# Optimization experiments

Hardware: AMD Instinct MI355X
Metric: run time of the kernel (lower is better)

## Reference

```python
import jax, jax.numpy as jnp
import numpy as np

GROUPS = 32
HEADS = 8
EPS = 1e-5

def setup_inputs() -> dict:
    key = jax.random.key(0)
    ks = jax.random.split(key, 5)
    C = 512
    x = jax.random.normal(ks[0], (8, C, 32, 32), dtype=jnp.float32)
    gn_w = jnp.ones((C,), dtype=jnp.float32)
    gn_b = jnp.zeros((C,), dtype=jnp.float32)
    qkv_w = jax.random.normal(ks[1], (3 * C, C), dtype=jnp.float32) * 0.02
    qkv_b = jnp.zeros((3 * C,), dtype=jnp.float32)
    proj_w = jax.random.normal(ks[2], (C, C), dtype=jnp.float32) * 0.02
    proj_b = jnp.zeros((C,), dtype=jnp.float32)
    return {"x": x, "gn_w": gn_w, "gn_b": gn_b, "qkv_w": qkv_w,
            "qkv_b": qkv_b, "proj_w": proj_w, "proj_b": proj_b}

def reference(x, gn_w, gn_b, qkv_w, qkv_b, proj_w, proj_b):
    B, C, H, W = x.shape
    d = C // HEADS
    # GroupNorm(32, C)
    xg = x.reshape(B, GROUPS, C // GROUPS, H, W)
    mean = xg.mean(axis=(2, 3, 4), keepdims=True)
    var = xg.var(axis=(2, 3, 4), keepdims=True)
    h = ((xg - mean) * jax.lax.rsqrt(var + EPS)).reshape(B, C, H, W)
    h = h * gn_w[None, :, None, None] + gn_b[None, :, None, None]
    # 1x1 conv QKV == channel matmul
    qkv = jnp.einsum('bchw,oc->bohw', h, qkv_w) + qkv_b[None, :, None, None]
    qkv = qkv.reshape(B, 3, HEADS, d, H * W)
    q, k, v = qkv[:, 0], qkv[:, 1], qkv[:, 2]  # [B, heads, d, HW]
    scale = d ** (-0.5)
    # weight[b,h,q,k] = sum_d q[b,h,d,q] * k[b,h,d,k] * scale
    attn = jax.nn.softmax(jnp.einsum('bhdq,bhdk->bhqk', q, k) * scale, axis=-1)
    # out[b,h,d,q] = sum_k v[b,h,d,k] * attn[b,h,q,k]
    out = jnp.einsum('bhdk,bhqk->bhdq', v, attn).reshape(B, C, H, W)
    out = jnp.einsum('bchw,oc->bohw', out, proj_w) + proj_b[None, :, None, None]
    return out + x
```

## Files before the change

### kernel.cpp

```cpp
#include <hip/hip_runtime.h>
#include <math.h>

#define B_    8
#define C_    512
#define HW_   1024
#define O3_   1536
#define HEADS_ 8
#define D_    64
#define G_    32
#define CPG_  16
#define EPS_  1e-5f
#define M_TOT 8192

#define QSCALE (0.125f * 1.44269504088896f)

typedef __bf16 bf16x8 __attribute__((ext_vector_type(8)));
typedef __bf16 bf16x4 __attribute__((ext_vector_type(4)));
typedef float  f32x4  __attribute__((ext_vector_type(4)));

__device__ __forceinline__ void async_copy16(void* lds, const void* g) {
  __builtin_amdgcn_global_load_lds(
      (const __attribute__((address_space(1))) unsigned int*)g,
      (__attribute__((address_space(3))) unsigned int*)lds, 16, 0, 0);
}

__global__ __launch_bounds__(256) void k_gn(const float* __restrict__ x,
                                            const float* __restrict__ gw,
                                            const float* __restrict__ gb,
                                            __bf16* __restrict__ h,
                                            const float* __restrict__ qw,
                                            const float* __restrict__ pw,
                                            __bf16* __restrict__ qwb,
                                            __bf16* __restrict__ pwb) {
  __shared__ float red[10];
  __shared__ __bf16 T[16 * 1030];
  if (blockIdx.x >= B_ * G_) {
    int i = (blockIdx.x - B_ * G_) * 256 + threadIdx.x;
    if (i < O3_ * C_) qwb[i] = (__bf16)qw[i];
    if (i < C_ * C_)  pwb[i] = (__bf16)pw[i];
    return;
  }
  int bg = blockIdx.x;
  int b = bg >> 5, g = bg & 31;
  const float* xg = x + ((size_t)(b * C_) + g * CPG_) * HW_;
  int tid = threadIdx.x;

  float s = 0.f, ss = 0.f;
  for (int i = tid; i < CPG_ * HW_; i += 256) {
    float v = xg[i];
    s += v; ss += v * v;
  }
  for (int off = 32; off > 0; off >>= 1) {
    s  += __shfl_down(s, off, 64);
    ss += __shfl_down(ss, off, 64);
  }
  int wv = tid >> 6;
  if ((tid & 63) == 0) { red[wv] = s; red[4 + wv] = ss; }
  __syncthreads();
  if (tid == 0) {
    float S  = red[0] + red[1] + red[2] + red[3];
    float SS = red[4] + red[5] + red[6] + red[7];
    float mean = S / (float)(CPG_ * HW_);
    float var  = SS / (float)(CPG_ * HW_) - mean * mean;
    red[8] = mean;
    red[9] = rsqrtf(var + EPS_);
  }
  __syncthreads();
  float mean = red[8], rstd = red[9];

  for (int i = tid; i < CPG_ * HW_; i += 256) {
    int c = i >> 10, hw = i & 1023;
    float ga = gw[g * CPG_ + c], be = gb[g * CPG_ + c];
    float v = xg[i];
    T[c * 1030 + hw] = (__bf16)((v - mean) * rstd * ga + be);
  }
  __syncthreads();

  __bf16* hb = h + (size_t)b * HW_ * C_ + g * CPG_;
  for (int j = tid; j < CPG_ * HW_; j += 256) {
    int hw = j >> 4, c = j & 15;
    hb[(size_t)hw * C_ + c] = T[c * 1030 + hw];
  }
}

#define BK 64
__device__ __forceinline__ void gemm128_core(const __bf16* __restrict__ aBase,
                                             const __bf16* __restrict__ bBase,
                                             __bf16* As, __bf16* Bs,
                                             f32x4 acc[4][4]) {
  int t = threadIdx.x;
  int lane = t & 63;
  int l16 = lane & 15, quad = lane >> 4;
  int wv = t >> 6;
  int wm = (wv >> 1) * 64, wn = (wv & 1) * 64;

  int rsub = lane >> 3;
  int chunk = (lane & 7) ^ rsub;
  const __bf16* ag = aBase + (size_t)(wv * 32 + rsub) * C_ + chunk * 8;
  const __bf16* bg = bBase + (size_t)(wv * 32 + rsub) * C_ + chunk * 8;
  __bf16* la = As + wv * 2048 + lane * 8;
  __bf16* lb = Bs + wv * 2048 + lane * 8;
  int sw = l16 & 7;

  for (int k0 = 0; k0 < C_; k0 += BK) {
#pragma unroll
    for (int s = 0; s < 4; s++) {
      async_copy16(la + s * 512, ag + (size_t)(s * 8) * C_ + k0);
      async_copy16(lb + s * 512, bg + (size_t)(s * 8) * C_ + k0);
    }
    __syncthreads();
#pragma unroll
    for (int h = 0; h < 2; h++) {
      bf16x8 af[4], bf[4];
#pragma unroll
      for (int i = 0; i < 4; i++) {
        af[i] = *(const bf16x8*)(As + (wm + i * 16 + l16) * BK +
                                 ((h * 4 + quad) ^ sw) * 8);
        bf[i] = *(const bf16x8*)(Bs + (wn + i * 16 + l16) * BK +
                                 ((h * 4 + quad) ^ sw) * 8);
      }
#pragma unroll
      for (int i = 0; i < 4; i++)
#pragma unroll
        for (int j = 0; j < 4; j++)
          acc[i][j] = __builtin_amdgcn_mfma_f32_16x16x32_bf16(af[i], bf[j],
                                                              acc[i][j], 0, 0, 0);
    }
    __syncthreads();
  }
}

__global__ __launch_bounds__(256) void k_qkv(const __bf16* __restrict__ h,
                                             const __bf16* __restrict__ w,
                                             const float* __restrict__ bias,
                                             __bf16* __restrict__ y,
                                             __bf16* __restrict__ vT) {
  __shared__ __align__(16) __bf16 As[128 * BK];
  __shared__ __align__(16) __bf16 Bs[128 * BK];
  int m0 = blockIdx.x * 128, n0 = blockIdx.y * 128;
  f32x4 acc[4][4];
#pragma unroll
  for (int i = 0; i < 4; i++)
#pragma unroll
    for (int j = 0; j < 4; j++) acc[i][j] = f32x4{0.f, 0.f, 0.f, 0.f};
  gemm128_core(h + (size_t)m0 * C_, w + (size_t)n0 * C_, As, Bs, acc);

  int lane = threadIdx.x & 63, wv = threadIdx.x >> 6;
  int l16 = lane & 15, quad = lane >> 4;
  int wm = (wv >> 1) * 64, wn = (wv & 1) * 64;

  if (n0 >= 2 * C_) {
    int bb = m0 >> 10;
    int tokBase = (m0 & 1023) + wm + quad * 4;
#pragma unroll
    for (int j = 0; j < 4; j++) {
      int n = n0 + wn + j * 16 + l16;
      int c = n - 2 * C_;
      float bv = bias[n];
      __bf16* vrow = vT + ((size_t)(bb * C_) + c) * HW_;
#pragma unroll
      for (int i = 0; i < 4; i++) {
        bf16x4 pk;
#pragma unroll
        for (int r = 0; r < 4; r++) pk[r] = (__bf16)(acc[i][j][r] + bv);
        *(bf16x4*)(vrow + tokBase + i * 16) = pk;
      }
    }
  } else {
    float sc = (n0 < C_) ? QSCALE : 1.0f;
#pragma unroll
    for (int j = 0; j < 4; j++) {
      int n = n0 + wn + j * 16 + l16;
      float bv = bias[n];
#pragma unroll
      for (int i = 0; i < 4; i++)
#pragma unroll
        for (int r = 0; r < 4; r++) {
          int m = m0 + wm + i * 16 + quad * 4 + r;
          y[(size_t)m * O3_ + n] = (__bf16)((acc[i][j][r] + bv) * sc);
        }
    }
  }
}

__global__ __launch_bounds__(256) void k_attn(const __bf16* __restrict__ y,
                                              const __bf16* __restrict__ vT,
                                              __bf16* __restrict__ ao) {
  __shared__ __align__(16) __bf16 Ks[128 * 64];
  __shared__ __align__(16) __bf16 Vt[64 * 128];
  __shared__ __align__(16) __bf16 Pp[4][32 * 136];
  int hd = blockIdx.x, b = blockIdx.y, qt = blockIdx.z;
  int t = threadIdx.x;
  int wv = t >> 6, lane = t & 63, l16 = lane & 15, quad = lane >> 4;
  int q0 = qt * 128 + wv * 32;

  const __bf16* base = y + (size_t)(b * HW_) * O3_ + hd * D_;
  const __bf16* kg = base + C_;
  const __bf16* vtg = vT + ((size_t)(b * C_) + hd * D_) * HW_;

  bf16x8 qb[2][2];
#pragma unroll
  for (int qg = 0; qg < 2; qg++)
#pragma unroll
    for (int dh = 0; dh < 2; dh++)
      qb[qg][dh] = *(const bf16x8*)(base + (size_t)(q0 + qg * 16 + l16) * O3_ +
                                    dh * 32 + quad * 8);

  int kRowSub = lane >> 3;
  int kChunk = (lane & 7) ^ (kRowSub & 7);

  float l_run[2] = {0.f, 0.f};
  f32x4 o_acc[4][2];
#pragma unroll
  for (int dt = 0; dt < 4; dt++)
#pragma unroll
    for (int qg = 0; qg < 2; qg++) o_acc[dt][qg] = f32x4{0.f, 0.f, 0.f, 0.f};

  for (int kt = 0; kt < HW_; kt += 128) {
#pragma unroll
    for (int s = 0; s < 4; s++) {
      int row = wv * 32 + s * 8 + kRowSub;
      async_copy16(Ks + (wv * 32 + s * 8) * 64 + lane * 8,
                   kg + (size_t)(kt + row) * O3_ + kChunk * 8);
    }
#pragma unroll
    for (int s = 0; s < 4; s++) {
      int row = wv * 16 + s * 4 + (lane >> 4);
      int c2 = (lane & 15) ^ (row & 15);
      async_copy16(Vt + (wv * 16 + s * 4) * 128 + lane * 8,
                   vtg + (size_t)row * HW_ + kt + c2 * 8);
    }
    __syncthreads();

    f32x4 st[8][2];
#pragma unroll
    for (int tt = 0; tt < 8; tt++) {
      int row = tt * 16 + l16;
      bf16x8 ka0 = *(const bf16x8*)(&Ks[row * 64 + ((quad) ^ (l16 & 7)) * 8]);
      bf16x8 ka1 = *(const bf16x8*)(&Ks[row * 64 + ((4 + quad) ^ (l16 & 7)) * 8]);
      f32x4 z = {0.f, 0.f, 0.f, 0.f};
      st[tt][0] = __builtin_amdgcn_mfma_f32_16x16x32_bf16(ka0, qb[0][0], z, 0, 0, 0);
      st[tt][0] = __builtin_amdgcn_mfma_f32_16x16x32_bf16(ka1, qb[0][1], st[tt][0], 0, 0, 0);
      st[tt][1] = __builtin_amdgcn_mfma_f32_16x16x32_bf16(ka0, qb[1][0], z, 0, 0, 0);
      st[tt][1] = __builtin_amdgcn_mfma_f32_16x16x32_bf16(ka1, qb[1][1], st[tt][1], 0, 0, 0);
    }

#pragma unroll
    for (int qg = 0; qg < 2; qg++) {
      float rs = 0.f;
#pragma unroll
      for (int tt = 0; tt < 8; tt++)
#pragma unroll
        for (int r = 0; r < 4; r++) {
          float e = exp2f(st[tt][qg][r]);
          st[tt][qg][r] = e;
          rs += e;
        }
      l_run[qg] += rs;
    }

#pragma unroll
    for (int qg = 0; qg < 2; qg++)
#pragma unroll
      for (int tt = 0; tt < 8; tt++) {
        bf16x4 pk;
#pragma unroll
        for (int r = 0; r < 4; r++) pk[r] = (__bf16)st[tt][qg][r];
        *(bf16x4*)(&Pp[wv][(qg * 16 + l16) * 136 + tt * 16 + quad * 4]) = pk;
      }
    asm volatile("s_waitcnt lgkmcnt(0)" ::: "memory");

#pragma unroll
    for (int kh = 0; kh < 4; kh++) {
      bf16x8 pb0 = *(const bf16x8*)(&Pp[wv][l16 * 136 + kh * 32 + quad * 8]);
      bf16x8 pb1 = *(const bf16x8*)(&Pp[wv][(16 + l16) * 136 + kh * 32 + quad * 8]);
#pragma unroll
      for (int dt = 0; dt < 4; dt++) {
        int vpos = ((kh * 4 + quad) ^ l16) * 8;
        bf16x8 va = *(const bf16x8*)(&Vt[(dt * 16 + l16) * 128 + vpos]);
        o_acc[dt][0] = __builtin_amdgcn_mfma_f32_16x16x32_bf16(va, pb0, o_acc[dt][0], 0, 0, 0);
        o_acc[dt][1] = __builtin_amdgcn_mfma_f32_16x16x32_bf16(va, pb1, o_acc[dt][1], 0, 0, 0);
      }
    }
    __syncthreads();
  }

#pragma unroll
  for (int qg = 0; qg < 2; qg++) {
    l_run[qg] += __shfl_xor(l_run[qg], 16, 64);
    l_run[qg] += __shfl_xor(l_run[qg], 32, 64);
  }
  float inv0 = 1.f / l_run[0], inv1 = 1.f / l_run[1];

#pragma unroll
  for (int dt = 0; dt < 4; dt++) {
    bf16x4 p0, p1;
#pragma unroll
    for (int r = 0; r < 4; r++) {
      p0[r] = (__bf16)(o_acc[dt][0][r] * inv0);
      p1[r] = (__bf16)(o_acc[dt][1][r] * inv1);
    }
    int ch = hd * D_ + dt * 16 + quad * 4;
    *(bf16x4*)(ao + (size_t)(b * HW_ + q0 + l16) * C_ + ch) = p0;
    *(bf16x4*)(ao + (size_t)(b * HW_ + q0 + 16 + l16) * C_ + ch) = p1;
  }
}

__global__ __launch_bounds__(256) void k_proj(const __bf16* __restrict__ ao,
                                              const __bf16* __restrict__ w,
                                              const float* __restrict__ bias,
                                              const float* __restrict__ x,
                                              float* __restrict__ out) {
  __shared__ __align__(16) __bf16 As[128 * BK];
  __shared__ __align__(16) __bf16 Bs[128 * BK];
  int n0 = blockIdx.x * 128, m0 = blockIdx.y * 128;
  f32x4 acc[4][4];
#pragma unroll
  for (int i = 0; i < 4; i++)
#pragma unroll
    for (int j = 0; j < 4; j++) acc[i][j] = f32x4{0.f, 0.f, 0.f, 0.f};
  gemm128_core(w + (size_t)m0 * C_, ao + (size_t)n0 * C_, As, Bs, acc);

  int lane = threadIdx.x & 63, wv = threadIdx.x >> 6;
  int l16 = lane & 15, quad = lane >> 4;
  int wm = (wv >> 1) * 64, wn = (wv & 1) * 64;
#pragma unroll
  for (int i = 0; i < 4; i++)
#pragma unroll
    for (int r = 0; r < 4; r++) {
      int o = m0 + wm + i * 16 + quad * 4 + r;
      float bv = bias[o];
#pragma unroll
      for (int j = 0; j < 4; j++) {
        int n = n0 + wn + j * 16 + l16;
        int b = n >> 10, hw = n & 1023;
        size_t idx = ((size_t)(b * C_ + o)) * HW_ + hw;
        out[idx] = acc[i][j][r] + bv + x[idx];
      }
    }
}

extern "C" void kernel_launch(void* const* d_in, const int* in_sizes, int n_in,
                              void* d_out, int out_size, void* d_ws, size_t ws_size,
                              hipStream_t stream) {
  const float* x      = (const float*)d_in[0];
  const float* gn_w   = (const float*)d_in[1];
  const float* gn_b   = (const float*)d_in[2];
  const float* qkv_w  = (const float*)d_in[3];
  const float* qkv_b  = (const float*)d_in[4];
  const float* proj_w = (const float*)d_in[5];
  const float* proj_b = (const float*)d_in[6];
  float* out = (float*)d_out;

  char* ws = (char*)d_ws;
  __bf16* h   = (__bf16*)(ws);
  __bf16* qwb = (__bf16*)(ws + 8388608);
  __bf16* pwb = (__bf16*)(ws + 8388608 + 1572864);
  __bf16* yq  = (__bf16*)(ws + 8388608 + 1572864 + 524288);
  __bf16* ao  = (__bf16*)(ws + 8388608 + 1572864 + 524288 + 25165824);
  __bf16* vT  = (__bf16*)(ws + 8388608 + 1572864 + 524288 + 25165824 + 8388608);

  int cvtBlocks = (O3_ * C_ + 255) / 256;
  k_gn  <<<B_ * G_ + cvtBlocks, 256, 0, stream>>>(x, gn_w, gn_b, h,
                                                  qkv_w, proj_w, qwb, pwb);
  k_qkv <<<dim3(M_TOT / 128, O3_ / 128, 1), 256, 0, stream>>>(h, qwb, qkv_b, yq, vT);
  k_attn<<<dim3(HEADS_, B_, 8), 256, 0, stream>>>(yq, vT, ao);
  k_proj<<<dim3(M_TOT / 128, C_ / 128, 1), 256, 0, stream>>>(ao, pwb, proj_b, x, out);
  (void)in_sizes; (void)n_in; (void)out_size; (void)ws_size;
}
```

Baseline: 170.2 us.

## Double-buffer K/V tiles in attention and process scores in 32-key chunks

Attention K and V tiles are now double-buffered in LDS, so the next tile's async global-to-LDS loads are issued before the current tile is computed, overlapping memory latency with MFMA work. The score/exp/PV stage is restructured to work in 32-key sub-chunks, which shrinks the per-wave P scratch buffer and the live register set for scores. It also switches to the raw hardware exp2 builtin. LDS use grows from the doubled K/V buffers, which could reduce blocks per CU, and there are more waitcnt points per tile.

```diff
diff --git a/kernel.cpp b/kernel.cpp
--- a/kernel.cpp
+++ b/kernel.cpp
@@ -186,9 +186,9 @@
 __global__ __launch_bounds__(256) void k_attn(const __bf16* __restrict__ y,
                                               const __bf16* __restrict__ vT,
                                               __bf16* __restrict__ ao) {
-  __shared__ __align__(16) __bf16 Ks[128 * 64];
-  __shared__ __align__(16) __bf16 Vt[64 * 128];
-  __shared__ __align__(16) __bf16 Pp[4][32 * 136];
+  __shared__ __align__(16) __bf16 Ks[2][128 * 64];
+  __shared__ __align__(16) __bf16 Vt[2][64 * 128];
+  __shared__ __align__(16) __bf16 Pp[4][32 * 36];
   int hd = blockIdx.x, b = blockIdx.y, qt = blockIdx.z;
   int t = threadIdx.x;
   int wv = t >> 6, lane = t & 63, l16 = lane & 15, quad = lane >> 4;
@@ -209,80 +209,86 @@
   int kRowSub = lane >> 3;
   int kChunk = (lane & 7) ^ (kRowSub & 7);
 
-  float l_run[2] = {0.f, 0.f};
-  f32x4 o_acc[4][2];
-#pragma unroll
-  for (int dt = 0; dt < 4; dt++)
-#pragma unroll
-    for (int qg = 0; qg < 2; qg++) o_acc[dt][qg] = f32x4{0.f, 0.f, 0.f, 0.f};
-
-  for (int kt = 0; kt < HW_; kt += 128) {
+  auto stage = [&](int kt, int bi) {
 #pragma unroll
     for (int s = 0; s < 4; s++) {
       int row = wv * 32 + s * 8 + kRowSub;
-      async_copy16(Ks + (wv * 32 + s * 8) * 64 + lane * 8,
+      async_copy16(&Ks[bi][(wv * 32 + s * 8) * 64 + lane * 8],
                    kg + (size_t)(kt + row) * O3_ + kChunk * 8);
     }
 #pragma unroll
     for (int s = 0; s < 4; s++) {
       int row = wv * 16 + s * 4 + (lane >> 4);
       int c2 = (lane & 15) ^ (row & 15);
-      async_copy16(Vt + (wv * 16 + s * 4) * 128 + lane * 8,
+      async_copy16(&Vt[bi][(wv * 16 + s * 4) * 128 + lane * 8],
                    vtg + (size_t)row * HW_ + kt + c2 * 8);
     }
-    __syncthreads();
-
-    f32x4 st[8][2];
-#pragma unroll
-    for (int tt = 0; tt < 8; tt++) {
-      int row = tt * 16 + l16;
-      bf16x8 ka0 = *(const bf16x8*)(&Ks[row * 64 + ((quad) ^ (l16 & 7)) * 8]);
-      bf16x8 ka1 = *(const bf16x8*)(&Ks[row * 64 + ((4 + quad) ^ (l16 & 7)) * 8]);
-      f32x4 z = {0.f, 0.f, 0.f, 0.f};
-      st[tt][0] = __builtin_amdgcn_mfma_f32_16x16x32_bf16(ka0, qb[0][0], z, 0, 0, 0);
-      st[tt][0] = __builtin_amdgcn_mfma_f32_16x16x32_bf16(ka1, qb[0][1], st[tt][0], 0, 0, 0);
-      st[tt][1] = __builtin_amdgcn_mfma_f32_16x16x32_bf16(ka0, qb[1][0], z, 0, 0, 0);
-      st[tt][1] = __builtin_amdgcn_mfma_f32_16x16x32_bf16(ka1, qb[1][1], st[tt][1], 0, 0, 0);
-    }
-
-#pragma unroll
-    for (int qg = 0; qg < 2; qg++) {
-      float rs = 0.f;
-#pragma unroll
-      for (int tt = 0; tt < 8; tt++)
-#pragma unroll
-        for (int r = 0; r < 4; r++) {
-          float e = exp2f(st[tt][qg][r]);
-          st[tt][qg][r] = e;
-          rs += e;
+  };
+
+  float l_run[2] = {0.f, 0.f};
+  f32x4 o_acc[4][2];
+#pragma unroll
+  for (int dt = 0; dt < 4; dt++)
+#pragma unroll
+    for (int qg = 0; qg < 2; qg++) o_acc[dt][qg] = f32x4{0.f, 0.f, 0.f, 0.f};
+
+  stage(0, 0);
+
+  for (int step = 0; step < 8; step++) {
+    int bi = step & 1;
+    asm volatile("s_waitcnt vmcnt(0)\n\ts_barrier" ::: "memory");
+    if (step < 7) stage((step + 1) * 128, bi ^ 1);
+
+    const __bf16* ks = Ks[bi];
+    const __bf16* vs = Vt[bi];
+#pragma unroll
+    for (int kh = 0; kh < 4; kh++) {
+      f32x4 st[2][2];
+#pragma unroll
+      for (int tti = 0; tti < 2; tti++) {
+        int row = (kh * 2 + tti) * 16 + l16;
+        bf16x8 ka0 = *(const bf16x8*)(&ks[row * 64 + ((quad) ^ (l16 & 7)) * 8]);
+        bf16x8 ka1 = *(const bf16x8*)(&ks[row * 64 + ((4 + quad) ^ (l16 & 7)) * 8]);
+        f32x4 z = {0.f, 0.f, 0.f, 0.f};
+        st[tti][0] = __builtin_amdgcn_mfma_f32_16x16x32_bf16(ka0, qb[0][0], z, 0, 0, 0);
+        st[tti][0] = __builtin_amdgcn_mfma_f32_16x16x32_bf16(ka1, qb[0][1], st[tti][0], 0, 0, 0);
+        st[tti][1] = __builtin_amdgcn_mfma_f32_16x16x32_bf16(ka0, qb[1][0], z, 0, 0, 0);
+        st[tti][1] = __builtin_amdgcn_mfma_f32_16x16x32_bf16(ka1, qb[1][1], st[tti][1], 0, 0, 0);
+      }
+#pragma unroll
+      for (int qg = 0; qg < 2; qg++) {
+        float rs = 0.f;
+#pragma unroll
+        for (int tti = 0; tti < 2; tti++)
+#pragma unroll
+          for (int r = 0; r < 4; r++) {
+            float e = __builtin_amdgcn_exp2f(st[tti][qg][r]);
+            st[tti][qg][r] = e;
+            rs += e;
+          }
+        l_run[qg] += rs;
+      }
+#pragma unroll
+      for (int qg = 0; qg < 2; qg++)
+#pragma unroll
+        for (int tti = 0; tti < 2; tti++) {
+          bf16x4 pk;
+#pragma unroll
+          for (int r = 0; r < 4; r++) pk[r] = (__bf16)st[tti][qg][r];
+          *(bf16x4*)(&Pp[wv][(qg * 16 + l16) * 36 + tti * 16 + quad * 4]) = pk;
         }
-      l_run[qg] += rs;
-    }
-
-#pragma unroll
-    for (int qg = 0; qg < 2; qg++)
-#pragma unroll
-      for (int tt = 0; tt < 8; tt++) {
-        bf16x4 pk;
-#pragma unroll
-        for (int r = 0; r < 4; r++) pk[r] = (__bf16)st[tt][qg][r];
-        *(bf16x4*)(&Pp[wv][(qg * 16 + l16) * 136 + tt * 16 + quad * 4]) = pk;
-      }
-    asm volatile("s_waitcnt lgkmcnt(0)" ::: "memory");
-
-#pragma unroll
-    for (int kh = 0; kh < 4; kh++) {
-      bf16x8 pb0 = *(const bf16x8*)(&Pp[wv][l16 * 136 + kh * 32 + quad * 8]);
-      bf16x8 pb1 = *(const bf16x8*)(&Pp[wv][(16 + l16) * 136 + kh * 32 + quad * 8]);
+      asm volatile("s_waitcnt lgkmcnt(0)" ::: "memory");
+      bf16x8 pb0 = *(const bf16x8*)(&Pp[wv][l16 * 36 + quad * 8]);
+      bf16x8 pb1 = *(const bf16x8*)(&Pp[wv][(16 + l16) * 36 + quad * 8]);
 #pragma unroll
       for (int dt = 0; dt < 4; dt++) {
         int vpos = ((kh * 4 + quad) ^ l16) * 8;
-        bf16x8 va = *(const bf16x8*)(&Vt[(dt * 16 + l16) * 128 + vpos]);
+        bf16x8 va = *(const bf16x8*)(&vs[(dt * 16 + l16) * 128 + vpos]);
         o_acc[dt][0] = __builtin_amdgcn_mfma_f32_16x16x32_bf16(va, pb0, o_acc[dt][0], 0, 0, 0);
         o_acc[dt][1] = __builtin_amdgcn_mfma_f32_16x16x32_bf16(va, pb1, o_acc[dt][1], 0, 0, 0);
       }
     }
-    __syncthreads();
+    asm volatile("s_barrier" ::: "memory");
   }
 
 #pragma unroll
```

Result: faster. 166.7 us (-2.1%).
